# Kernel tuning notes

Measured on AMD Instinct MI355X. Metric: run time of the kernel, lower is better.

The kernel has to match this reference:

```python
import jax, jax.numpy as jnp
import numpy as np

HEADS = 8
DIM_HEAD = 64
SCALE = DIM_HEAD ** -0.5


def setup_inputs() -> dict:
    key = jax.random.key(0)
    ks = jax.random.split(key, 8)
    B, Nq, Nk, D = 4, 1024, 2048, 512
    inner = HEADS * DIM_HEAD  # 512
    x = jax.random.normal(ks[0], (B, Nq, D), dtype=jnp.float32)
    context = jax.random.normal(ks[1], (B, Nk, D), dtype=jnp.float32)
    bias = jax.random.normal(ks[2], (B, Nq, Nk), dtype=jnp.float32)
    s = D ** -0.5
    Wq = jax.random.normal(ks[3], (inner, D), dtype=jnp.float32) * s
    Wk = jax.random.normal(ks[4], (inner, D), dtype=jnp.float32) * s
    Wv = jax.random.normal(ks[5], (inner, D), dtype=jnp.float32) * s
    Wo = jax.random.normal(ks[6], (D, inner), dtype=jnp.float32) * s
    bo = jnp.zeros((D,), dtype=jnp.float32)
    return {"x": x, "context": context, "bias": bias,
            "Wq": Wq, "Wk": Wk, "Wv": Wv, "Wo": Wo, "bo": bo}


def reference(x, context, bias, Wq, Wk, Wv, Wo, bo):
    B, Nq, _ = x.shape
    # torch Linear: y = x @ W.T ; reshape (h d) -> b h n d
    q = (x @ Wq.T).reshape(B, Nq, HEADS, DIM_HEAD).transpose(0, 2, 1, 3)
    k = (context @ Wk.T).reshape(B, -1, HEADS, DIM_HEAD).transpose(0, 2, 1, 3)
    v = (context @ Wv.T).reshape(B, -1, HEADS, DIM_HEAD).transpose(0, 2, 1, 3)
    # explicit-score fallback path (bias supplied)
    scores = jnp.einsum('bhqd,bhkd->bhqk', q, k) * SCALE
    scores = scores + bias[:, None, :, :]  # 3D bias -> (B,1,Nq,Nk)
    attn = jax.nn.softmax(scores, axis=-1)
    out = jnp.einsum('bhqk,bhkd->bhqd', attn, v)
    out = out.transpose(0, 2, 1, 3).reshape(B, Nq, HEADS * DIM_HEAD)
    return out @ Wo.T + bo
```

## Files before the change

### kernel.cpp

```cpp
#include <hip/hip_runtime.h>

#define H 8
#define DH 64
#define NQ 1024
#define NK 2048
#define DIN 512
#define B 4
#define KSPLIT 2
#define KRANGE (NK / KSPLIT)
#define KTILES (KRANGE / 64)
#define BHNQ (B * H * NQ)

typedef __bf16 bf16;
typedef __bf16 bf16x8 __attribute__((ext_vector_type(8)));
typedef __bf16 bf16x4 __attribute__((ext_vector_type(4)));
typedef float floatx4 __attribute__((ext_vector_type(4)));

__device__ inline void gload16(const void* g, void* l) {
  __builtin_amdgcn_global_load_lds(
      (const __attribute__((address_space(1))) void*)g,
      (__attribute__((address_space(3))) void*)l, 16, 0, 0);
}

__global__ void cvt_all(const float* __restrict__ bias,
                        const float* __restrict__ wq, const float* __restrict__ wk,
                        const float* __restrict__ wv, const float* __restrict__ wo,
                        bf16* bias16, bf16* wqb, bf16* wkb, bf16* wvb, bf16* wob) {
  long i = ((long)blockIdx.x * 256 + threadIdx.x) * 4;
  const float* s; bf16* d; long o;
  if (i < 8388608)      { s = bias; d = bias16; o = i; }
  else if (i < 8650752) { s = wq;  d = wqb; o = i - 8388608; }
  else if (i < 8912896) { s = wk;  d = wkb; o = i - 8650752; }
  else if (i < 9175040) { s = wv;  d = wvb; o = i - 8912896; }
  else                  { s = wo;  d = wob; o = i - 9175040; }
  float4 f = *(const float4*)(s + o);
  bf16x4 v = { (bf16)f.x, (bf16)f.y, (bf16)f.z, (bf16)f.w };
  *(bf16x4*)(d + o) = v;
}

__global__ __launch_bounds__(256) void gemm_qkv(
    const float* __restrict__ x, const float* __restrict__ ctx,
    const bf16* __restrict__ wqb, const bf16* __restrict__ wkb, const bf16* __restrict__ wvb,
    bf16* __restrict__ qb, bf16* __restrict__ kb, bf16* __restrict__ vtb) {
  const int which = blockIdx.z;
  if (which == 0 && blockIdx.y >= 64) return;
  const float* A32 = (which == 0) ? x : ctx;
  const bf16* W = (which == 0) ? wqb : ((which == 1) ? wkb : wvb);
  bf16* outb = (which == 0) ? qb : ((which == 1) ? kb : vtb);
  const int logT = (which == 0) ? 10 : 11;
  const float scale = (which == 0) ? 0.125f : 1.0f;
  const bool vmode = (which == 2);

  __shared__ bf16 Al[2][64 * 32];
  __shared__ bf16 Bl[2][128 * 32];
  const int t = threadIdx.x;
  const int lane = t & 63, w = t >> 6;
  const int ln = lane & 15, quad = lane >> 4;
  const int wm = (w >> 1) * 32, wn = (w & 1) * 64;
  const int rowBase = blockIdx.y * 64;
  const int colBase = blockIdx.x * 128;

  floatx4 acc[2][4] = {};
  const int rA = t >> 2, oA = (t & 3) * 8;
  const int c0 = t, c1 = t + 256;
  const int rB0 = c0 >> 2, oB0 = (c0 & 3) * 8;
  const int rB1 = c1 >> 2, oB1 = (c1 & 3) * 8;
  const float* Ab = A32 + (size_t)(rowBase + rA) * DIN + oA;
  const bf16* Wb = W + (size_t)colBase * DIN;

  float4 la0, la1;
  la0 = *(const float4*)(Ab + 0);
  la1 = *(const float4*)(Ab + 4);
  {
    bf16x8 v = {(bf16)la0.x, (bf16)la0.y, (bf16)la0.z, (bf16)la0.w,
                (bf16)la1.x, (bf16)la1.y, (bf16)la1.z, (bf16)la1.w};
    *(bf16x8*)&Al[0][t * 8] = v;
  }
  gload16(Wb + (size_t)rB0 * DIN + oB0, &Bl[0][c0 * 8]);
  gload16(Wb + (size_t)rB1 * DIN + oB1, &Bl[0][c1 * 8]);
  __syncthreads();

  for (int kk = 0; kk < 16; kk++) {
    const int cur = kk & 1, nxt = cur ^ 1;
    const int k1 = (kk + 1) * 32;
    if (kk < 15) {
      la0 = *(const float4*)(Ab + k1);
      la1 = *(const float4*)(Ab + k1 + 4);
      gload16(Wb + (size_t)rB0 * DIN + k1 + oB0, &Bl[nxt][c0 * 8]);
      gload16(Wb + (size_t)rB1 * DIN + k1 + oB1, &Bl[nxt][c1 * 8]);
    }
    bf16x8 af[2], bfr[4];
#pragma unroll
    for (int i = 0; i < 2; i++)
      af[i] = *(const bf16x8*)&Al[cur][(wm + i * 16 + ln) * 32 + quad * 8];
#pragma unroll
    for (int j = 0; j < 4; j++)
      bfr[j] = *(const bf16x8*)&Bl[cur][(wn + j * 16 + ln) * 32 + quad * 8];
    if (!vmode) {
#pragma unroll
      for (int i = 0; i < 2; i++)
#pragma unroll
        for (int j = 0; j < 4; j++)
          acc[i][j] = __builtin_amdgcn_mfma_f32_16x16x32_bf16(af[i], bfr[j], acc[i][j], 0, 0, 0);
    } else {
#pragma unroll
      for (int i = 0; i < 2; i++)
#pragma unroll
        for (int j = 0; j < 4; j++)
          acc[i][j] = __builtin_amdgcn_mfma_f32_16x16x32_bf16(bfr[j], af[i], acc[i][j], 0, 0, 0);
    }
    if (kk < 15) {
      bf16x8 v = {(bf16)la0.x, (bf16)la0.y, (bf16)la0.z, (bf16)la0.w,
                  (bf16)la1.x, (bf16)la1.y, (bf16)la1.z, (bf16)la1.w};
      *(bf16x8*)&Al[nxt][t * 8] = v;
    }
    __syncthreads();
  }

  const int T = 1 << logT;
#pragma unroll
  for (int i = 0; i < 2; i++)
#pragma unroll
    for (int j = 0; j < 4; j++)
#pragma unroll
      for (int r = 0; r < 4; r++) {
        if (!vmode) {
          const int m = rowBase + wm + i * 16 + quad * 4 + r;
          const int n = colBase + wn + j * 16 + ln;
          const float v = acc[i][j][r] * scale;
          const int bb = m >> logT, tok = m & (T - 1);
          const int hh = n >> 6, d = n & 63;
          outb[((((size_t)(bb * H + hh)) << logT) + tok) * DH + d] = (bf16)v;
        } else {
          const int dg = colBase + wn + j * 16 + quad * 4 + r;
          const int m = rowBase + wm + i * 16 + ln;
          const int bb = m >> logT, tok = m & (T - 1);
          const int hh = dg >> 6, d = dg & 63;
          outb[(((size_t)(bb * H + hh) * DH + d) << logT) + tok] = (bf16)acc[i][j][r];
        }
      }
}

__global__ __launch_bounds__(128) void attn_fwd(
    const bf16* __restrict__ q, const bf16* __restrict__ k,
    const bf16* __restrict__ vt, const bf16* __restrict__ bias16,
    bf16* __restrict__ op0, bf16* __restrict__ op1, float* __restrict__ lpart) {
  __shared__ bf16 KL[64 * 64];
  __shared__ bf16 VL[64 * 64];
  __shared__ bf16 BL[64 * 64];
  __shared__ bf16 Pl[2][2][16 * 64];
  const int tid = threadIdx.x;
  const int lane = tid & 63, w = tid >> 6;
  const int ln = lane & 15, quad = lane >> 4;
  const int hh = blockIdx.y;
  const int b = blockIdx.z >> 1, ks = blockIdx.z & 1;
  const int q0 = blockIdx.x * 64;
  const int k0 = ks * KRANGE;
  const size_t bh = (size_t)b * H + hh;
  const bf16* qp = q + bh * NQ * DH;
  const bf16* kp = k + bh * NK * DH;
  const bf16* vp = vt + bh * DH * NK;
  const bf16* bb = bias16 + ((size_t)b * NQ + q0) * NK;

  bf16x8 qf[2][2];
#pragma unroll
  for (int s = 0; s < 2; s++)
#pragma unroll
    for (int kc = 0; kc < 2; kc++)
      qf[s][kc] = *(const bf16x8*)(qp + (size_t)(q0 + w * 32 + s * 16 + ln) * DH + kc * 32 + quad * 8);

  floatx4 o[2][4] = {};
  floatx4 lac[2] = {};
  const bf16x8 ones = {(bf16)1.f, (bf16)1.f, (bf16)1.f, (bf16)1.f,
                       (bf16)1.f, (bf16)1.f, (bf16)1.f, (bf16)1.f};
  constexpr float L2E = 1.44269504f;
  constexpr float OFF = 34.6246810f;

  for (int tt = 0; tt < KTILES; tt++) {
    const int nk0 = k0 + tt * 64;
#pragma unroll
    for (int s = 0; s < 4; s++) {
      const int i = s * 128 + tid;
      const int sr = i >> 3, sc = (i & 7) ^ (sr & 7);
      gload16(kp + (size_t)(nk0 + sr) * DH + sc * 8, &KL[i * 8]);
      gload16(vp + (size_t)sr * NK + nk0 + sc * 8, &VL[i * 8]);
      gload16(bb + (size_t)sr * NK + nk0 + sc * 8, &BL[i * 8]);
    }
    __syncthreads();

    floatx4 s4[2][4] = {};
#pragma unroll
    for (int j = 0; j < 4; j++)
#pragma unroll
      for (int kc = 0; kc < 2; kc++) {
        const int kr = j * 16 + ln;
        bf16x8 kf = *(const bf16x8*)&KL[kr * 64 + (((kc * 4 + quad) ^ (kr & 7)) * 8)];
        s4[0][j] = __builtin_amdgcn_mfma_f32_16x16x32_bf16(qf[0][kc], kf, s4[0][j], 0, 0, 0);
        s4[1][j] = __builtin_amdgcn_mfma_f32_16x16x32_bf16(qf[1][kc], kf, s4[1][j], 0, 0, 0);
      }

#pragma unroll
    for (int s = 0; s < 2; s++)
#pragma unroll
      for (int j = 0; j < 4; j++)
#pragma unroll
        for (int r = 0; r < 4; r++) {
          const int m = w * 32 + s * 16 + quad * 4 + r;
          const float bv = (float)BL[m * 64 + (((j * 2 + (ln >> 3)) ^ (m & 7)) * 8) + (ln & 7)];
          s4[s][j][r] = exp2f(fmaf(s4[s][j][r] + bv, L2E, -OFF));
        }

#pragma unroll
    for (int s = 0; s < 2; s++)
#pragma unroll
      for (int j = 0; j < 4; j++)
#pragma unroll
        for (int r = 0; r < 4; r++) {
          const int m = quad * 4 + r;
          Pl[w][s][m * 64 + (((j * 2 + (ln >> 3)) ^ (m & 7)) * 8) + (ln & 7)] = (bf16)s4[s][j][r];
        }
    asm volatile("s_waitcnt lgkmcnt(0)" ::: "memory");
    bf16x8 pf[2][2];
#pragma unroll
    for (int s = 0; s < 2; s++)
#pragma unroll
      for (int kc = 0; kc < 2; kc++)
        pf[s][kc] = *(const bf16x8*)&Pl[w][s][ln * 64 + (((kc * 4 + quad) ^ (ln & 7)) * 8)];

#pragma unroll
    for (int s = 0; s < 2; s++)
#pragma unroll
      for (int kc = 0; kc < 2; kc++)
        lac[s] = __builtin_amdgcn_mfma_f32_16x16x32_bf16(pf[s][kc], ones, lac[s], 0, 0, 0);

#pragma unroll
    for (int jn = 0; jn < 4; jn++)
#pragma unroll
      for (int kc = 0; kc < 2; kc++) {
        const int vr = jn * 16 + ln;
        bf16x8 vf = *(const bf16x8*)&VL[vr * 64 + (((kc * 4 + quad) ^ (vr & 7)) * 8)];
        o[0][jn] = __builtin_amdgcn_mfma_f32_16x16x32_bf16(pf[0][kc], vf, o[0][jn], 0, 0, 0);
        o[1][jn] = __builtin_amdgcn_mfma_f32_16x16x32_bf16(pf[1][kc], vf, o[1][jn], 0, 0, 0);
      }
    __syncthreads();
  }

#pragma unroll
  for (int s = 0; s < 2; s++) {
    bf16* op = (ks ? op1 : op0) +
               ((size_t)b * NQ + q0 + w * 32 + s * 16 + quad * 4) * DIN + hh * 64 + ln;
#pragma unroll
    for (int jn = 0; jn < 4; jn++)
#pragma unroll
      for (int r = 0; r < 4; r++)
        op[(size_t)r * DIN + jn * 16] = (bf16)o[s][jn][r];
    if (ln == 0) {
      float4 lv = {lac[s][0], lac[s][1], lac[s][2], lac[s][3]};
      *(float4*)&lpart[((size_t)ks * B * H + b * H + hh) * NQ + q0 + w * 32 + s * 16 + quad * 4] = lv;
    }
  }
}

__global__ __launch_bounds__(256) void gemm_out(
    const bf16* __restrict__ op0, const bf16* __restrict__ op1,
    const float* __restrict__ lp, const bf16* __restrict__ W,
    float* __restrict__ outf, const float* __restrict__ bo) {
  __shared__ bf16 Al[2][64 * 32];
  __shared__ bf16 Bl[2][128 * 32];
  const int t = threadIdx.x;
  const int lane = t & 63, w = t >> 6;
  const int ln = lane & 15, quad = lane >> 4;
  const int wm = (w >> 1) * 32, wn = (w & 1) * 64;
  const int rowBase = blockIdx.y * 64;
  const int colBase = blockIdx.x * 128;

  floatx4 acc[2][4] = {};
  const int rA = t >> 2, oA = (t & 3) * 8;
  const int c0 = t, c1 = t + 256;
  const int rB0 = c0 >> 2, oB0 = (c0 & 3) * 8;
  const int rB1 = c1 >> 2, oB1 = (c1 & 3) * 8;
  const int m0 = rowBase + rA;
  const bf16* Wb = W + (size_t)colBase * DIN;

  float linv0[8];
#pragma unroll
  for (int h = 0; h < 8; h++) {
    const int i0 = ((m0 >> 10) * H + h) * NQ + (m0 & 1023);
    linv0[h] = 1.0f / (lp[i0] + lp[BHNQ + i0]);
  }

#define STAGE_A(K0V, BUF)                                                      \
  {                                                                            \
    const float sA = linv0[(K0V) >> 6];                                        \
    bf16x8 u0 = *(const bf16x8*)(op0 + (size_t)m0 * DIN + (K0V) + oA);         \
    bf16x8 u1 = *(const bf16x8*)(op1 + (size_t)m0 * DIN + (K0V) + oA);         \
    bf16x8 v0;                                                                 \
    _Pragma("unroll")                                                          \
    for (int e = 0; e < 8; e++)                                                \
      v0[e] = (bf16)(((float)u0[e] + (float)u1[e]) * sA);                      \
    *(bf16x8*)&Al[BUF][t * 8] = v0;                                            \
  }

  STAGE_A(0, 0);
  gload16(Wb + (size_t)rB0 * DIN + oB0, &Bl[0][c0 * 8]);
  gload16(Wb + (size_t)rB1 * DIN + oB1, &Bl[0][c1 * 8]);
  __syncthreads();

#pragma unroll
  for (int kk = 0; kk < 16; kk++) {
    const int cur = kk & 1, nxt = cur ^ 1;
    if (kk < 15) {
      const int k1 = (kk + 1) * 32;
      STAGE_A(k1, nxt);
      gload16(Wb + (size_t)rB0 * DIN + k1 + oB0, &Bl[nxt][c0 * 8]);
      gload16(Wb + (size_t)rB1 * DIN + k1 + oB1, &Bl[nxt][c1 * 8]);
    }
    bf16x8 af[2], bfr[4];
#pragma unroll
    for (int i = 0; i < 2; i++)
      af[i] = *(const bf16x8*)&Al[cur][(wm + i * 16 + ln) * 32 + quad * 8];
#pragma unroll
    for (int j = 0; j < 4; j++)
      bfr[j] = *(const bf16x8*)&Bl[cur][(wn + j * 16 + ln) * 32 + quad * 8];
#pragma unroll
    for (int i = 0; i < 2; i++)
#pragma unroll
      for (int j = 0; j < 4; j++)
        acc[i][j] = __builtin_amdgcn_mfma_f32_16x16x32_bf16(af[i], bfr[j], acc[i][j], 0, 0, 0);
    __syncthreads();
  }
#undef STAGE_A

#pragma unroll
  for (int i = 0; i < 2; i++)
#pragma unroll
    for (int j = 0; j < 4; j++)
#pragma unroll
      for (int r = 0; r < 4; r++) {
        const int m = rowBase + wm + i * 16 + quad * 4 + r;
        const int n = colBase + wn + j * 16 + ln;
        outf[(size_t)m * DIN + n] = acc[i][j][r] + bo[n];
      }
}

extern "C" void kernel_launch(void* const* d_in, const int* in_sizes, int n_in,
                              void* d_out, int out_size, void* d_ws, size_t ws_size,
                              hipStream_t stream) {
  const float* x    = (const float*)d_in[0];
  const float* ctx  = (const float*)d_in[1];
  const float* bias = (const float*)d_in[2];
  const float* Wq   = (const float*)d_in[3];
  const float* Wk   = (const float*)d_in[4];
  const float* Wv   = (const float*)d_in[5];
  const float* Wo   = (const float*)d_in[6];
  const float* bo   = (const float*)d_in[7];
  float* out = (float*)d_out;

  char* p = (char*)d_ws;
  bf16* bias16 = (bf16*)(p + 0);
  bf16* wqb  = (bf16*)(p + 16777216);
  bf16* wkb  = (bf16*)(p + 17301504);
  bf16* wvb  = (bf16*)(p + 17825792);
  bf16* wob  = (bf16*)(p + 18350080);
  bf16* qb   = (bf16*)(p + 18874368);
  bf16* kb   = (bf16*)(p + 23068672);
  bf16* vtb  = (bf16*)(p + 31457280);
  bf16* op0  = (bf16*)(p + 39845888);
  bf16* op1  = (bf16*)(p + 44040192);
  float* lpart = (float*)(p + 48234496);

  cvt_all<<<9216, 256, 0, stream>>>(bias, Wq, Wk, Wv, Wo, bias16, wqb, wkb, wvb, wob);
  gemm_qkv<<<dim3(4, 128, 3), 256, 0, stream>>>(x, ctx, wqb, wkb, wvb, qb, kb, vtb);
  attn_fwd<<<dim3(NQ / 64, H, B * KSPLIT), 128, 0, stream>>>(qb, kb, vtb, bias16, op0, op1, lpart);
  gemm_out<<<dim3(4, 64), 256, 0, stream>>>(op0, op1, lpart, wob, out, bo);
}
```

Before: 201.5 us.

## Read fp32 bias directly in attention, drop bias conversion, split keys four ways

Removes the bias-to-bf16 conversion pass and instead loads fp32 bias straight from global memory into registers, using it as the MFMA accumulator initial value. This skips a full write and reread of the 32MB bias tensor and frees the LDS bias tile. KSPLIT goes from 2 to 4 for more parallelism, which means four partial output buffers and four partial row sums for gemm_out to combine. The cost is that bias is now read 8 times, once per head, as fp32 with strided scalar loads rather than once as bf16 via LDS.

Result: slower. 208.4 us (+3.5%).

```diff
diff --git a/kernel.cpp b/kernel.cpp
--- a/kernel.cpp
+++ b/kernel.cpp
@@ -6,7 +6,7 @@
 #define NK 2048
 #define DIN 512
 #define B 4
-#define KSPLIT 2
+#define KSPLIT 4
 #define KRANGE (NK / KSPLIT)
 #define KTILES (KRANGE / 64)
 #define BHNQ (B * H * NQ)
@@ -22,17 +22,15 @@
       (__attribute__((address_space(3))) void*)l, 16, 0, 0);
 }
 
-__global__ void cvt_all(const float* __restrict__ bias,
-                        const float* __restrict__ wq, const float* __restrict__ wk,
-                        const float* __restrict__ wv, const float* __restrict__ wo,
-                        bf16* bias16, bf16* wqb, bf16* wkb, bf16* wvb, bf16* wob) {
-  long i = ((long)blockIdx.x * 256 + threadIdx.x) * 4;
-  const float* s; bf16* d; long o;
-  if (i < 8388608)      { s = bias; d = bias16; o = i; }
-  else if (i < 8650752) { s = wq;  d = wqb; o = i - 8388608; }
-  else if (i < 8912896) { s = wk;  d = wkb; o = i - 8650752; }
-  else if (i < 9175040) { s = wv;  d = wvb; o = i - 8912896; }
-  else                  { s = wo;  d = wob; o = i - 9175040; }
+__global__ void cvt_w(const float* __restrict__ wq, const float* __restrict__ wk,
+                      const float* __restrict__ wv, const float* __restrict__ wo,
+                      bf16* wqb, bf16* wkb, bf16* wvb, bf16* wob) {
+  int i = (blockIdx.x * 256 + threadIdx.x) * 4;
+  const float* s; bf16* d; int o;
+  if (i < 262144)      { s = wq; d = wqb; o = i; }
+  else if (i < 524288) { s = wk; d = wkb; o = i - 262144; }
+  else if (i < 786432) { s = wv; d = wvb; o = i - 524288; }
+  else                 { s = wo; d = wob; o = i - 786432; }
   float4 f = *(const float4*)(s + o);
   bf16x4 v = { (bf16)f.x, (bf16)f.y, (bf16)f.z, (bf16)f.w };
   *(bf16x4*)(d + o) = v;
@@ -143,24 +141,23 @@
 
 __global__ __launch_bounds__(128) void attn_fwd(
     const bf16* __restrict__ q, const bf16* __restrict__ k,
-    const bf16* __restrict__ vt, const bf16* __restrict__ bias16,
-    bf16* __restrict__ op0, bf16* __restrict__ op1, float* __restrict__ lpart) {
+    const bf16* __restrict__ vt, const float* __restrict__ bias,
+    bf16* __restrict__ opb, float* __restrict__ lpart) {
   __shared__ bf16 KL[64 * 64];
   __shared__ bf16 VL[64 * 64];
-  __shared__ bf16 BL[64 * 64];
   __shared__ bf16 Pl[2][2][16 * 64];
   const int tid = threadIdx.x;
   const int lane = tid & 63, w = tid >> 6;
   const int ln = lane & 15, quad = lane >> 4;
   const int hh = blockIdx.y;
-  const int b = blockIdx.z >> 1, ks = blockIdx.z & 1;
+  const int b = blockIdx.z >> 2, ks = blockIdx.z & 3;
   const int q0 = blockIdx.x * 64;
   const int k0 = ks * KRANGE;
   const size_t bh = (size_t)b * H + hh;
   const bf16* qp = q + bh * NQ * DH;
   const bf16* kp = k + bh * NK * DH;
   const bf16* vp = vt + bh * DH * NK;
-  const bf16* bb = bias16 + ((size_t)b * NQ + q0) * NK;
+  const float* bp = bias + ((size_t)b * NQ + q0 + w * 32 + quad * 4) * NK + ln;
 
   bf16x8 qf[2][2];
 #pragma unroll
@@ -184,11 +181,25 @@
       const int sr = i >> 3, sc = (i & 7) ^ (sr & 7);
       gload16(kp + (size_t)(nk0 + sr) * DH + sc * 8, &KL[i * 8]);
       gload16(vp + (size_t)sr * NK + nk0 + sc * 8, &VL[i * 8]);
-      gload16(bb + (size_t)sr * NK + nk0 + sc * 8, &BL[i * 8]);
-    }
+    }
+    float bc[2][4][4];
+#pragma unroll
+    for (int s = 0; s < 2; s++)
+#pragma unroll
+      for (int j = 0; j < 4; j++)
+#pragma unroll
+        for (int r = 0; r < 4; r++)
+          bc[s][j][r] = bp[(size_t)(s * 16 + r) * NK + nk0 + j * 16];
     __syncthreads();
 
-    floatx4 s4[2][4] = {};
+    floatx4 s4[2][4];
+#pragma unroll
+    for (int s = 0; s < 2; s++)
+#pragma unroll
+      for (int j = 0; j < 4; j++) {
+        s4[s][j][0] = bc[s][j][0]; s4[s][j][1] = bc[s][j][1];
+        s4[s][j][2] = bc[s][j][2]; s4[s][j][3] = bc[s][j][3];
+      }
 #pragma unroll
     for (int j = 0; j < 4; j++)
 #pragma unroll
@@ -204,11 +215,8 @@
 #pragma unroll
       for (int j = 0; j < 4; j++)
 #pragma unroll
-        for (int r = 0; r < 4; r++) {
-          const int m = w * 32 + s * 16 + quad * 4 + r;
-          const float bv = (float)BL[m * 64 + (((j * 2 + (ln >> 3)) ^ (m & 7)) * 8) + (ln & 7)];
-          s4[s][j][r] = exp2f(fmaf(s4[s][j][r] + bv, L2E, -OFF));
-        }
+        for (int r = 0; r < 4; r++)
+          s4[s][j][r] = exp2f(fmaf(s4[s][j][r], L2E, -OFF));
 
 #pragma unroll
     for (int s = 0; s < 2; s++)
@@ -247,7 +255,7 @@
 
 #pragma unroll
   for (int s = 0; s < 2; s++) {
-    bf16* op = (ks ? op1 : op0) +
+    bf16* op = opb + (size_t)ks * B * NQ * DIN +
                ((size_t)b * NQ + q0 + w * 32 + s * 16 + quad * 4) * DIN + hh * 64 + ln;
 #pragma unroll
     for (int jn = 0; jn < 4; jn++)
@@ -262,9 +270,8 @@
 }
 
 __global__ __launch_bounds__(256) void gemm_out(
-    const bf16* __restrict__ op0, const bf16* __restrict__ op1,
-    const float* __restrict__ lp, const bf16* __restrict__ W,
-    float* __restrict__ outf, const float* __restrict__ bo) {
+    const bf16* __restrict__ opb, const float* __restrict__ lp,
+    const bf16* __restrict__ W, float* __restrict__ outf, const float* __restrict__ bo) {
   __shared__ bf16 Al[2][64 * 32];
   __shared__ bf16 Bl[2][128 * 32];
   const int t = threadIdx.x;
@@ -286,18 +293,22 @@
 #pragma unroll
   for (int h = 0; h < 8; h++) {
     const int i0 = ((m0 >> 10) * H + h) * NQ + (m0 & 1023);
-    linv0[h] = 1.0f / (lp[i0] + lp[BHNQ + i0]);
+    linv0[h] = 1.0f / (lp[i0] + lp[BHNQ + i0] + lp[2 * BHNQ + i0] + lp[3 * BHNQ + i0]);
   }
 
 #define STAGE_A(K0V, BUF)                                                      \
   {                                                                            \
     const float sA = linv0[(K0V) >> 6];                                        \
-    bf16x8 u0 = *(const bf16x8*)(op0 + (size_t)m0 * DIN + (K0V) + oA);         \
-    bf16x8 u1 = *(const bf16x8*)(op1 + (size_t)m0 * DIN + (K0V) + oA);         \
+    const size_t base = (size_t)m0 * DIN + (K0V) + oA;                         \
+    bf16x8 u0 = *(const bf16x8*)(opb + base);                                  \
+    bf16x8 u1 = *(const bf16x8*)(opb + (size_t)B * NQ * DIN + base);           \
+    bf16x8 u2 = *(const bf16x8*)(opb + (size_t)2 * B * NQ * DIN + base);       \
+    bf16x8 u3 = *(const bf16x8*)(opb + (size_t)3 * B * NQ * DIN + base);       \
     bf16x8 v0;                                                                 \
     _Pragma("unroll")                                                          \
     for (int e = 0; e < 8; e++)                                                \
-      v0[e] = (bf16)(((float)u0[e] + (float)u1[e]) * sA);                      \
+      v0[e] = (bf16)((((float)u0[e] + (float)u1[e]) +                          \
+                      ((float)u2[e] + (float)u3[e])) * sA);                    \
     *(bf16x8*)&Al[BUF][t * 8] = v0;                                            \
   }
 
@@ -357,20 +368,18 @@
   float* out = (float*)d_out;
 
   char* p = (char*)d_ws;
-  bf16* bias16 = (bf16*)(p + 0);
-  bf16* wqb  = (bf16*)(p + 16777216);
-  bf16* wkb  = (bf16*)(p + 17301504);
-  bf16* wvb  = (bf16*)(p + 17825792);
-  bf16* wob  = (bf16*)(p + 18350080);
-  bf16* qb   = (bf16*)(p + 18874368);
-  bf16* kb   = (bf16*)(p + 23068672);
-  bf16* vtb  = (bf16*)(p + 31457280);
-  bf16* op0  = (bf16*)(p + 39845888);
-  bf16* op1  = (bf16*)(p + 44040192);
-  float* lpart = (float*)(p + 48234496);
-
-  cvt_all<<<9216, 256, 0, stream>>>(bias, Wq, Wk, Wv, Wo, bias16, wqb, wkb, wvb, wob);
+  bf16* wqb  = (bf16*)(p + 0);
+  bf16* wkb  = (bf16*)(p + 524288);
+  bf16* wvb  = (bf16*)(p + 1048576);
+  bf16* wob  = (bf16*)(p + 1572864);
+  bf16* qb   = (bf16*)(p + 2097152);
+  bf16* kb   = (bf16*)(p + 6291456);
+  bf16* vtb  = (bf16*)(p + 14680064);
+  bf16* opb  = (bf16*)(p + 23068672);
+  float* lpart = (float*)(p + 39845888);
+
+  cvt_w<<<1024, 256, 0, stream>>>(Wq, Wk, Wv, Wo, wqb, wkb, wvb, wob);
   gemm_qkv<<<dim3(4, 128, 3), 256, 0, stream>>>(x, ctx, wqb, wkb, wvb, qb, kb, vtb);
-  attn_fwd<<<dim3(NQ / 64, H, B * KSPLIT), 128, 0, stream>>>(qb, kb, vtb, bias16, op0, op1, lpart);
-  gemm_out<<<dim3(4, 64), 256, 0, stream>>>(op0, op1, lpart, wob, out, bo);
-}
+  attn_fwd<<<dim3(NQ / 64, H, B * KSPLIT), 128, 0, stream>>>(qb, kb, vtb, bias, opb, lpart);
+  gemm_out<<<dim3(4, 64), 256, 0, stream>>>(opb, lpart, wob, out, bo);
+}
```
